# Optimization experiments

Measured on AMD Instinct MI355X. Metric: run time of the kernel, lower is better.

The kernel has to match this reference:

```python
import jax, jax.numpy as jnp
import numpy as np
import math

B, LQ, LK, D = 8, 2048, 2048, 1024  # hidden_dim = O_dim = D


def setup_inputs() -> dict:
    key = jax.random.key(0)
    ks = jax.random.split(key, 9)
    s = 1.0 / math.sqrt(D)
    return {
        "key": jax.random.normal(ks[0], (B, LK, D), dtype=jnp.float32),
        "query": jax.random.normal(ks[1], (B, LQ, D), dtype=jnp.float32),
        "mask": jax.random.randint(ks[2], (B, LK), 0, 2, dtype=jnp.int32),
        "Wq": jax.random.uniform(ks[3], (D, D), jnp.float32, -s, s),
        "bq": jax.random.uniform(ks[4], (D,), jnp.float32, -s, s),
        "Wk": jax.random.uniform(ks[5], (D, D), jnp.float32, -s, s),
        "bk": jax.random.uniform(ks[6], (D,), jnp.float32, -s, s),
        "Wv": jax.random.uniform(ks[7], (D, D), jnp.float32, -s, s),
        "bv": jax.random.uniform(ks[8], (D,), jnp.float32, -s, s),
    }


def reference(key, query, mask, Wq, bq, Wk, bk, Wv, bv):
    # Linear projections (torch nn.Linear: x @ W.T + b)
    q = jnp.einsum("bld,hd->blh", query, Wq) + bq          # [B, LQ, H]
    k = jnp.einsum("bld,hd->blh", key, Wk) + bk            # [B, LK, H]
    # Quirk of original module: values Linear is applied to the PROJECTED key
    v = jnp.einsum("blh,oh->blo", k, Wv) + bv              # [B, LK, O]
    score = jnp.einsum("bqh,bkh->bqk", q, k) / math.sqrt(D)
    # mask_score: mask [B, LK] -> [B, 1, LK], fill zeros with -1e9
    score = jnp.where(mask[:, None, :] == 0, jnp.float32(-1e9), score)
    score = jax.nn.softmax(score, axis=-1)
    # dropout in eval mode = identity; NaN cleanup preserved
    score = jnp.where(jnp.isnan(score), jnp.float32(0.0), score)
    output = jnp.einsum("bqk,bko->bqo", score, v)
    return output, score
```

## Files before the change

### kernel.cpp

```cpp
#include <hip/hip_runtime.h>
#include <cstdint>

#define DDIM 1024
#define LQN  2048
#define LKN  2048
#define BBAT 8


typedef short bf16x8 __attribute__((ext_vector_type(8)));
typedef float f32x4  __attribute__((ext_vector_type(4)));

__device__ __forceinline__ unsigned short f2bf(float f) {
    union { float f; unsigned int i; } x; x.f = f;
    unsigned int r = (x.i + 0x7fffu + ((x.i >> 16) & 1u)) >> 16;
    return (unsigned short)r;
}
__device__ __forceinline__ bf16x8 cvt8(const float* p) {
    float4 x0 = *(const float4*)p;
    float4 x1 = *(const float4*)(p + 4);
    bf16x8 r;
    r[0] = (short)f2bf(x0.x); r[1] = (short)f2bf(x0.y);
    r[2] = (short)f2bf(x0.z); r[3] = (short)f2bf(x0.w);
    r[4] = (short)f2bf(x1.x); r[5] = (short)f2bf(x1.y);
    r[6] = (short)f2bf(x1.z); r[7] = (short)f2bf(x1.w);
    return r;
}

__device__ __forceinline__ void gl2lds16(const void* g, void* l) {
    __builtin_amdgcn_global_load_lds(
        reinterpret_cast<const __attribute__((address_space(1))) void*>(
            reinterpret_cast<uintptr_t>(g)),
        reinterpret_cast<__attribute__((address_space(3))) void*>(
            (unsigned)reinterpret_cast<uintptr_t>(l)),
        16, 0, 0);
}

__global__ __launch_bounds__(256)
void cast_bf16(const float* __restrict__ in, unsigned short* __restrict__ out,
               long n8)
{
    long i = (long)blockIdx.x * blockDim.x + threadIdx.x;
    const long stride = (long)gridDim.x * blockDim.x;
    for (; i < n8; i += stride)
        *(bf16x8*)(out + i * 8) = cvt8(in + i * 8);
}

template<int MODE>
__global__ __launch_bounds__(256)
void gemm_nt(const unsigned short* __restrict__ A,
             const unsigned short* __restrict__ B,
             const float* __restrict__ bias,
             const int* __restrict__ mask,
             void* __restrict__ out)
{
    constexpr int K   = (MODE == 3) ? LKN : DDIM;
    constexpr int LDA = K;
    constexpr int LDB = K;

    __shared__ unsigned short lA[128 * 32];
    __shared__ unsigned short lB[128 * 32];

    const int t    = threadIdx.x;
    const int lane = t & 63;
    const int wave = t >> 6;
    const int wm   = wave >> 1;
    const int wn   = wave & 1;

    const int bm = blockIdx.y;
    const int bn = blockIdx.x;
    const int z  = blockIdx.z;

    const unsigned short* Ap = A;
    const unsigned short* Bp = B;
    if (MODE == 2) { Ap += (long)z * LQN * DDIM; Bp += (long)z * LKN * DDIM; }
    if (MODE == 3) { Ap += (long)z * LQN * LKN;  Bp += (long)z * DDIM * LKN; }

    const int srow = t >> 2;
    const int skk  = (t & 3) * 8;
    const unsigned short* ga0 = Ap + (long)(bm * 128 + srow) * LDA + skk;
    const unsigned short* ga1 = ga0 + 64L * LDA;
    const unsigned short* gb0 = Bp + (long)(bn * 128 + srow) * LDB + skk;
    const unsigned short* gb1 = gb0 + 64L * LDB;
    unsigned short* lAw = lA + wave * 512;
    unsigned short* lBw = lB + wave * 512;

    f32x4 acc[4][4];
    #pragma unroll
    for (int i = 0; i < 4; ++i)
        #pragma unroll
        for (int j = 0; j < 4; ++j)
            acc[i][j] = (f32x4)(0.0f);

    const int quad = lane >> 4;
    const int l15  = lane & 15;

    for (int k0 = 0; k0 < K; k0 += 32) {
        __syncthreads();
        gl2lds16(ga0 + k0, lAw);
        gl2lds16(ga1 + k0, lAw + 2048);
        gl2lds16(gb0 + k0, lBw);
        gl2lds16(gb1 + k0, lBw + 2048);
        __syncthreads();

        bf16x8 af[4], bfv[4];
        #pragma unroll
        for (int i = 0; i < 4; ++i)
            af[i] = *(const bf16x8*)&lA[(wm * 64 + i * 16 + l15) * 32 + quad * 8];
        #pragma unroll
        for (int j = 0; j < 4; ++j)
            bfv[j] = *(const bf16x8*)&lB[(wn * 64 + j * 16 + l15) * 32 + quad * 8];

        #pragma unroll
        for (int i = 0; i < 4; ++i)
            #pragma unroll
            for (int j = 0; j < 4; ++j)
                acc[i][j] = __builtin_amdgcn_mfma_f32_16x16x32_bf16(
                    af[i], bfv[j], acc[i][j], 0, 0, 0);
    }

    #pragma unroll
    for (int i = 0; i < 4; ++i) {
        #pragma unroll
        for (int j = 0; j < 4; ++j) {
            const int grow = bm * 128 + wm * 64 + i * 16 + quad * 4;
            const int gcol = bn * 128 + wn * 64 + j * 16 + l15;
            if (MODE == 0) {
                const float bc = bias[gcol];
                #pragma unroll
                for (int r = 0; r < 4; ++r)
                    ((unsigned short*)out)[(long)(grow + r) * DDIM + gcol] =
                        f2bf(acc[i][j][r] + bc);
            } else if (MODE == 1) {
                const int b2 = gcol >> 11;
                const int lk = gcol & 2047;
                #pragma unroll
                for (int r = 0; r < 4; ++r) {
                    const float bc = bias[grow + r];
                    ((unsigned short*)out)[(long)b2 * DDIM * LKN +
                                           (long)(grow + r) * LKN + lk] =
                        f2bf(acc[i][j][r] + bc);
                }
            } else if (MODE == 2) {
                const int mv = mask[z * LKN + gcol];
                #pragma unroll
                for (int r = 0; r < 4; ++r) {
                    float v = acc[i][j][r] * 0.03125f;
                    if (mv == 0) v = -1e9f;
                    ((float*)out)[(long)z * LQN * LKN +
                                  (long)(grow + r) * LKN + gcol] = v;
                }
            } else {
                #pragma unroll
                for (int r = 0; r < 4; ++r)
                    ((float*)out)[(long)z * LQN * DDIM +
                                  (long)(grow + r) * DDIM + gcol] = acc[i][j][r];
            }
        }
    }
}

__global__ __launch_bounds__(256)
void softmax_rows(float* __restrict__ P, unsigned short* __restrict__ Pb)
{
    const int t = threadIdx.x;
    const long base = (long)blockIdx.x * LKN + t * 8;

    float4 r0 = *(const float4*)&P[base];
    float4 r1 = *(const float4*)&P[base + 4];
    float v[8] = { r0.x, r0.y, r0.z, r0.w, r1.x, r1.y, r1.z, r1.w };

    float m = -3.0e38f;
    #pragma unroll
    for (int i = 0; i < 8; ++i) m = fmaxf(m, v[i]);
    #pragma unroll
    for (int off = 32; off >= 1; off >>= 1) m = fmaxf(m, __shfl_xor(m, off, 64));
    __shared__ float redm[4];
    if ((t & 63) == 0) redm[t >> 6] = m;
    __syncthreads();
    m = fmaxf(fmaxf(redm[0], redm[1]), fmaxf(redm[2], redm[3]));

    float s = 0.0f;
    #pragma unroll
    for (int i = 0; i < 8; ++i) { v[i] = __expf(v[i] - m); s += v[i]; }
    #pragma unroll
    for (int off = 32; off >= 1; off >>= 1) s += __shfl_xor(s, off, 64);
    __shared__ float reds[4];
    if ((t & 63) == 0) reds[t >> 6] = s;
    __syncthreads();
    s = reds[0] + reds[1] + reds[2] + reds[3];

    const float inv = 1.0f / s;
    r0.x = v[0] * inv; r0.y = v[1] * inv; r0.z = v[2] * inv; r0.w = v[3] * inv;
    r1.x = v[4] * inv; r1.y = v[5] * inv; r1.z = v[6] * inv; r1.w = v[7] * inv;
    *(float4*)&P[base]     = r0;
    *(float4*)&P[base + 4] = r1;

    bf16x8 pb;
    pb[0] = (short)f2bf(r0.x); pb[1] = (short)f2bf(r0.y);
    pb[2] = (short)f2bf(r0.z); pb[3] = (short)f2bf(r0.w);
    pb[4] = (short)f2bf(r1.x); pb[5] = (short)f2bf(r1.y);
    pb[6] = (short)f2bf(r1.z); pb[7] = (short)f2bf(r1.w);
    *(bf16x8*)&Pb[base] = pb;
}

extern "C" void kernel_launch(void* const* d_in, const int* in_sizes, int n_in,
                              void* d_out, int out_size, void* d_ws, size_t ws_size,
                              hipStream_t stream)
{
    (void)in_sizes; (void)n_in; (void)out_size;

    const float* key   = (const float*)d_in[0];
    const float* query = (const float*)d_in[1];
    const int*   mask  = (const int*)d_in[2];
    const float* Wq    = (const float*)d_in[3];
    const float* bq    = (const float*)d_in[4];
    const float* Wk    = (const float*)d_in[5];
    const float* bk    = (const float*)d_in[6];
    const float* Wv    = (const float*)d_in[7];
    const float* bv    = (const float*)d_in[8];

    float* outO = (float*)d_out;
    float* outP = outO + (size_t)BBAT * LQN * DDIM;

    unsigned short* Wqb  = (unsigned short*)d_ws;
    unsigned short* Wkb  = Wqb + (size_t)DDIM * DDIM;
    unsigned short* Wvb  = Wkb + (size_t)DDIM * DDIM;
    unsigned short* gbuf = Wvb + (size_t)DDIM * DDIM;

    const size_t fixed = (size_t)3 * DDIM * DDIM * sizeof(unsigned short);
    const size_t perB  = ((size_t)LQN * LKN + (size_t)3 * LQN * DDIM) *
                         sizeof(unsigned short);
    size_t avail = (ws_size > fixed) ? (ws_size - fixed) : 0;
    int g = (int)(avail / perB);
    if (g > BBAT) g = BBAT;
    if (g < 1)    g = 1;

    dim3 blk(256, 1, 1);

    cast_bf16<<<dim3(512, 1, 1), blk, 0, stream>>>(Wq, Wqb, (long)DDIM * DDIM / 8);
    cast_bf16<<<dim3(512, 1, 1), blk, 0, stream>>>(Wk, Wkb, (long)DDIM * DDIM / 8);
    cast_bf16<<<dim3(512, 1, 1), blk, 0, stream>>>(Wv, Wvb, (long)DDIM * DDIM / 8);

    for (int b0 = 0; b0 < BBAT; b0 += g) {
        const int gl = (BBAT - b0 < g) ? (BBAT - b0) : g;

        unsigned short* regionA = gbuf;
        unsigned short* qc = regionA;
        unsigned short* kc = regionA + (size_t)gl * LQN * DDIM;
        unsigned short* Pb = regionA;
        unsigned short* Qp = regionA + (size_t)gl * LQN * LKN;
        unsigned short* Kp = Qp + (size_t)gl * LQN * DDIM;
        unsigned short* Vt = Kp + (size_t)gl * LKN * DDIM;

        cast_bf16<<<dim3(2048, 1, 1), blk, 0, stream>>>(
            query + (size_t)b0 * LQN * DDIM, qc, (long)gl * LQN * DDIM / 8);
        cast_bf16<<<dim3(2048, 1, 1), blk, 0, stream>>>(
            key + (size_t)b0 * LKN * DDIM, kc, (long)gl * LKN * DDIM / 8);

        gemm_nt<0><<<dim3(8, gl * 16, 1), blk, 0, stream>>>(qc, Wqb, bq, nullptr, Qp);

        gemm_nt<0><<<dim3(8, gl * 16, 1), blk, 0, stream>>>(kc, Wkb, bk, nullptr, Kp);

        gemm_nt<1><<<dim3(gl * 16, 8, 1), blk, 0, stream>>>(Wvb, Kp, bv, nullptr, Vt);

        gemm_nt<2><<<dim3(16, 16, gl), blk, 0, stream>>>(
            Qp, Kp, nullptr, mask + (size_t)b0 * LKN,
            outP + (size_t)b0 * LQN * LKN);

        softmax_rows<<<dim3(gl * LQN, 1, 1), blk, 0, stream>>>(
            outP + (size_t)b0 * LQN * LKN, Pb);

        gemm_nt<3><<<dim3(8, 16, gl), blk, 0, stream>>>(
            Pb, Vt, nullptr, nullptr, outO + (size_t)b0 * LQN * DDIM);
    }
}
```

Measured before the change: 752.7 us.

## Double-buffer LDS tiles in GEMM and remap block IDs across XCDs

The GEMM kernel now uses two LDS buffers and prefetches the next K-tile while MFMAs run on the current one, so there is one barrier per iteration instead of two. It also remaps linear block IDs so neighbouring tiles land on the same XCD, aiming for better L2 locality. In exchange it doubles LDS use per block, which may reduce occupancy.

```diff
diff --git a/kernel.cpp b/kernel.cpp
--- a/kernel.cpp
+++ b/kernel.cpp
@@ -56,9 +56,9 @@
     constexpr int K   = (MODE == 3) ? LKN : DDIM;
     constexpr int LDA = K;
     constexpr int LDB = K;
-
-    __shared__ unsigned short lA[128 * 32];
-    __shared__ unsigned short lB[128 * 32];
+    constexpr int NT  = K / 32;
+
+    __shared__ unsigned short lds[2][8192];
 
     const int t    = threadIdx.x;
     const int lane = t & 63;
@@ -66,8 +66,13 @@
     const int wm   = wave >> 1;
     const int wn   = wave & 1;
 
-    const int bm = blockIdx.y;
-    const int bn = blockIdx.x;
+    const int gx   = gridDim.x;
+    const int nwg  = gx * gridDim.y;
+    const int bid0 = blockIdx.y * gx + blockIdx.x;
+    const int bid  = ((nwg & 7) == 0) ? ((bid0 & 7) * (nwg >> 3) + (bid0 >> 3))
+                                      : bid0;
+    const int bm = bid / gx;
+    const int bn = bid % gx;
     const int z  = blockIdx.z;
 
     const unsigned short* Ap = A;
@@ -81,8 +86,7 @@
     const unsigned short* ga1 = ga0 + 64L * LDA;
     const unsigned short* gb0 = Bp + (long)(bn * 128 + srow) * LDB + skk;
     const unsigned short* gb1 = gb0 + 64L * LDB;
-    unsigned short* lAw = lA + wave * 512;
-    unsigned short* lBw = lB + wave * 512;
+    const int woff = wave * 512;
 
     f32x4 acc[4][4];
     #pragma unroll
@@ -94,21 +98,30 @@
     const int quad = lane >> 4;
     const int l15  = lane & 15;
 
-    for (int k0 = 0; k0 < K; k0 += 32) {
-        __syncthreads();
-        gl2lds16(ga0 + k0, lAw);
-        gl2lds16(ga1 + k0, lAw + 2048);
-        gl2lds16(gb0 + k0, lBw);
-        gl2lds16(gb1 + k0, lBw + 2048);
-        __syncthreads();
+#define STAGE(bufp, kk) do {                              \
+        gl2lds16(ga0 + (kk), (bufp) + woff);              \
+        gl2lds16(ga1 + (kk), (bufp) + woff + 2048);       \
+        gl2lds16(gb0 + (kk), (bufp) + 4096 + woff);       \
+        gl2lds16(gb1 + (kk), (bufp) + 4096 + woff + 2048);\
+    } while (0)
+
+    unsigned short* cur = &lds[0][0];
+    unsigned short* nxt = &lds[1][0];
+
+    STAGE(cur, 0);
+    __syncthreads();
+
+    for (int tt = 0; tt < NT; ++tt) {
+        if (tt + 1 < NT)
+            STAGE(nxt, (tt + 1) * 32);
 
         bf16x8 af[4], bfv[4];
         #pragma unroll
         for (int i = 0; i < 4; ++i)
-            af[i] = *(const bf16x8*)&lA[(wm * 64 + i * 16 + l15) * 32 + quad * 8];
+            af[i] = *(const bf16x8*)&cur[(wm * 64 + i * 16 + l15) * 32 + quad * 8];
         #pragma unroll
         for (int j = 0; j < 4; ++j)
-            bfv[j] = *(const bf16x8*)&lB[(wn * 64 + j * 16 + l15) * 32 + quad * 8];
+            bfv[j] = *(const bf16x8*)&cur[4096 + (wn * 64 + j * 16 + l15) * 32 + quad * 8];
 
         #pragma unroll
         for (int i = 0; i < 4; ++i)
@@ -116,7 +129,11 @@
             for (int j = 0; j < 4; ++j)
                 acc[i][j] = __builtin_amdgcn_mfma_f32_16x16x32_bf16(
                     af[i], bfv[j], acc[i][j], 0, 0, 0);
+
+        __syncthreads();
+        unsigned short* tmp = cur; cur = nxt; nxt = tmp;
     }
+#undef STAGE
 
     #pragma unroll
     for (int i = 0; i < 4; ++i) {
```

Result: faster. 721.0 us (-4.2%).
